# Performance work log

Hardware: AMD Instinct MI355X
Metric: run time of the kernel (lower is better)

Reference implementation:

```python
import jax, jax.numpy as jnp
import numpy as np

K = 4      # tagset_size - 2 (real emotion tags)
NT = 6     # tagset_size
START = 4
STOP = 5


def setup_inputs() -> dict:
    key = jax.random.key(0)
    ks = jax.random.split(key, 10)
    B, T = 2048, 2048
    feats = jax.random.normal(ks[0], (B, T, NT), dtype=jnp.float32)
    bias = jax.random.uniform(ks[1], (B, T), dtype=jnp.float32)        # bias_dict values in [0,1)
    tags = jax.random.randint(ks[2], (B, T), 0, K)                     # emotion labels only
    transitions = jax.random.normal(ks[3], (NT, NT), dtype=jnp.float32)
    transitions = transitions.at[START, :].set(-10000.0)
    transitions = transitions.at[:, STOP].set(-10000.0)
    w_shift_in = jax.random.normal(ks[4], (K,), dtype=jnp.float32)
    bias_no = jax.random.normal(ks[5], (1,), dtype=jnp.float32)
    bias_with = jax.random.normal(ks[6], (1,), dtype=jnp.float32)
    w_with_out = jax.random.normal(ks[7], (K,), dtype=jnp.float32)
    w_no_out = jax.random.normal(ks[8], (K,), dtype=jnp.float32)
    multiplier = jax.random.normal(ks[9], (K, K), dtype=jnp.float32)
    multiplier = multiplier.at[jnp.arange(K), jnp.arange(K)].set(-10000.0)
    return dict(feats=feats, bias=bias, tags=tags, transitions=transitions,
                w_shift_in=w_shift_in, bias_no=bias_no, bias_with=bias_with,
                w_with_out=w_with_out, w_no_out=w_no_out, multiplier=multiplier)


def reference(feats, bias, tags, transitions, w_shift_in, bias_no, bias_with,
              w_with_out, w_no_out, multiplier):
    """Batched neg_log_likelihood = forward_alg(feats) - score_sentence(feats, tags)."""
    B, T, _ = feats.shape
    # multiplier_softmax is over dim=0 (columns); diagonal overwritten with -1
    Mmod = jax.nn.softmax(multiplier, axis=0)
    Mmod = Mmod.at[jnp.arange(K), jnp.arange(K)].set(-1.0)

    # per-step transition gate, shape [B,T,K]; branch on bias > 0.5
    b = bias[..., None]
    gates = jnp.where(b > 0.5,
                      w_with_out * jnp.tanh(b * w_shift_in + bias_with),
                      w_no_out * jnp.tanh(b * w_shift_in + bias_no))

    # ---- forward algorithm (log-sum-exp DP over T, vectorized over B) ----
    init = jnp.full((B, NT), -10000.0, dtype=feats.dtype).at[:, START].set(0.0)
    feats_t = jnp.swapaxes(feats, 0, 1)   # [T,B,NT]
    gates_t = jnp.swapaxes(gates, 0, 1)   # [T,B,K]

    def step(alpha, x):
        f, g = x                                          # [B,NT], [B,K]
        blk = g[:, None, :] * Mmod[None, :, :]            # gate[prev] * Mmod[next,prev]
        Teff = transitions[None] + jnp.pad(blk, ((0, 0), (0, 2), (0, 2)))  # [B,NT,NT]
        alpha_new = f + jax.nn.logsumexp(alpha[:, None, :] + Teff, axis=2)
        return alpha_new, None

    alpha, _ = jax.lax.scan(step, init, (feats_t, gates_t))
    fwd_score = jax.nn.logsumexp(alpha + transitions[STOP][None, :], axis=1)  # [B]

    # ---- gold path score ----
    tags_ext = jnp.concatenate(
        [jnp.full((B, 1), START, dtype=tags.dtype), tags], axis=1)
    t0 = tags_ext[:, :-1]   # prev tag, [B,T]
    t1 = tags_ext[:, 1:]    # next tag, [B,T]
    base = transitions[t1, t0]
    Mext = jnp.pad(Mmod, ((0, 2), (0, 2)))
    gate_t0 = jnp.take_along_axis(gates, jnp.clip(t0, 0, K - 1)[..., None], axis=2)[..., 0]
    extra = jnp.where((t0 < K) & (t1 < K), gate_t0 * Mext[t1, t0], 0.0)
    emit = jnp.take_along_axis(feats, t1[..., None], axis=2)[..., 0]
    gold = jnp.sum(base + extra + emit, axis=1) + transitions[STOP, tags[:, -1]]

    return fwd_score - gold  # [B] per-dialog NLL
```

## Files before the change

### kernel.cpp

```cpp
#include <hip/hip_runtime.h>

#define BN 2048
#define TN 2048
#define BATCH 8
#define SLOT 24

__device__ __forceinline__ float ex2(float x){ return __builtin_amdgcn_exp2f(x); }
__device__ __forceinline__ float lg2(float x){ return __builtin_amdgcn_logf(x); }
__device__ __forceinline__ float rcpf(float x){ return __builtin_amdgcn_rcpf(x); }

constexpr float kLog2e = 1.4426950408889634f;
constexpr float kLn2   = 0.6931471805599453f;

__device__ __forceinline__ float fast_tanh(float x){
    float ax = fabsf(x);
    float e  = ex2(ax * (-2.0f * kLog2e));
    float t  = (1.0f - e) * rcpf(1.0f + e);
    return copysignf(t, x);
}

__device__ __forceinline__ float sel4(float v0, float v1, float v2, float v3, int idx){
    float r = (idx == 1) ? v1 : v0;
    r = (idx == 2) ? v2 : r;
    r = (idx == 3) ? v3 : r;
    return r;
}

template <int NCOL, bool CHUNK0, int TCH>
__device__ __forceinline__ void run_chunk(
    int b, int c,
    const float* __restrict__ feats, const float* __restrict__ bias,
    const int* __restrict__ tags,
    const float (&AL)[4][4], const float (&M)[4][4],
    const float (&wsv)[4], const float (&wwv)[4], const float (&wnv)[4],
    float bwc, float bnc, const float* sA, const float* sM,
    const float (&tc4)[4],
    float (&P)[4][NCOL], float (&lacc)[NCOL], float& gold, int& prev)
{
    const int t0c = c * TCH;
    #pragma unroll 1
    for (int bt = 0; bt < TCH / BATCH; ++bt) {
        const int t0 = t0c + bt * BATCH;
        float Fr[BATCH * 6];
        {
            const float4* fp4 = (const float4*)(feats + ((size_t)b * TN + t0) * 6);
            #pragma unroll
            for (int q = 0; q < BATCH * 6 / 4; ++q) {
                const float4 v = fp4[q];
                Fr[q*4+0] = v.x; Fr[q*4+1] = v.y; Fr[q*4+2] = v.z; Fr[q*4+3] = v.w;
            }
        }
        float Bv[BATCH];
        {
            const float4* bp4 = (const float4*)(bias + (size_t)b * TN + t0);
            #pragma unroll
            for (int q = 0; q < BATCH / 4; ++q) {
                const float4 v = bp4[q];
                Bv[q*4+0] = v.x; Bv[q*4+1] = v.y; Bv[q*4+2] = v.z; Bv[q*4+3] = v.w;
            }
        }
        int Tg[BATCH];
        {
            const int4* tp4 = (const int4*)(tags + (size_t)b * TN + t0);
            #pragma unroll
            for (int q = 0; q < BATCH / 4; ++q) {
                const int4 v = tp4[q];
                Tg[q*4+0] = v.x; Tg[q*4+1] = v.y; Tg[q*4+2] = v.z; Tg[q*4+3] = v.w;
            }
        }
        #pragma unroll
        for (int s = 0; s < BATCH; ++s) {
            const float fi0 = Fr[s*6+0], fi1 = Fr[s*6+1];
            const float fi2 = Fr[s*6+2], fi3 = Fr[s*6+3];
            if (CHUNK0 && bt == 0 && s == 0) {
                const float a0 = fi0 + tc4[0], a1 = fi1 + tc4[1];
                const float a2 = fi2 + tc4[2], a3 = fi3 + tc4[3];
                const float mx = fmaxf(fmaxf(a0, a1), fmaxf(a2, a3));
                P[0][0] = ex2((a0 - mx) * kLog2e);
                P[1][0] = ex2((a1 - mx) * kLog2e);
                P[2][0] = ex2((a2 - mx) * kLog2e);
                P[3][0] = ex2((a3 - mx) * kLog2e);
                lacc[0] = mx * kLog2e;
                const int tg0 = Tg[0];
                gold = sel4(tc4[0], tc4[1], tc4[2], tc4[3], tg0)
                     + sel4(fi0, fi1, fi2, fi3, tg0);
                prev = tg0;
                continue;
            }
            const float bv = Bv[s];
            const int tg = Tg[s];
            const bool hw = bv > 0.5f;
            const float bc = hw ? bwc : bnc;
            float g[4], gL[4];
            #pragma unroll
            for (int j = 0; j < 4; ++j) {
                float x = fmaf(bv, wsv[j], bc);
                g[j]  = (hw ? wwv[j] : wnv[j]) * fast_tanh(x);
                gL[j] = g[j] * kLog2e;
            }
            const float fiL[4] = { fi0 * kLog2e, fi1 * kLog2e,
                                   fi2 * kLog2e, fi3 * kLog2e };
            float nP[4][NCOL];
            #pragma unroll
            for (int i = 0; i < 4; ++i)
                #pragma unroll
                for (int j = 0; j < NCOL; ++j) nP[i][j] = 0.0f;
            #pragma unroll
            for (int k = 0; k < 4; ++k) {
                float Ek[4];
                #pragma unroll
                for (int i = 0; i < 4; ++i)
                    Ek[i] = ex2(fmaf(gL[k], M[i][k], fiL[i] + AL[i][k]));
                #pragma unroll
                for (int j = 0; j < NCOL; ++j) {
                    const float pk = P[k][j];
                    #pragma unroll
                    for (int i = 0; i < 4; ++i) nP[i][j] = fmaf(Ek[i], pk, nP[i][j]);
                }
            }
            #pragma unroll
            for (int i = 0; i < 4; ++i)
                #pragma unroll
                for (int j = 0; j < NCOL; ++j) P[i][j] = nP[i][j];

            const int idx = tg * 4 + prev;
            gold += sA[idx] + sel4(g[0], g[1], g[2], g[3], prev) * sM[idx]
                  + sel4(fi0, fi1, fi2, fi3, tg);
            prev = tg;

            if ((s & 3) == 3) {
                #pragma unroll
                for (int j = 0; j < NCOL; ++j) {
                    float m = fmaxf(fmaxf(P[0][j], P[1][j]), fmaxf(P[2][j], P[3][j]));
                    int ee = (int)((__float_as_uint(m) >> 23) & 255u) - 126;
                    float sc = __uint_as_float((unsigned)(127 - ee) << 23);
                    lacc[j] += (float)ee;
                    #pragma unroll
                    for (int i = 0; i < 4; ++i) P[i][j] *= sc;
                }
            }
        }
    }
}

template <int CCv>
__global__ void __launch_bounds__(256)
crf_phase1(const float* __restrict__ feats, const float* __restrict__ bias,
           const int* __restrict__ tags, const float* __restrict__ trans,
           const float* __restrict__ wsh, const float* __restrict__ bno,
           const float* __restrict__ bwi, const float* __restrict__ wwo,
           const float* __restrict__ wno, const float* __restrict__ mult,
           float* __restrict__ matAll)
{
    constexpr int TCHv = TN / CCv;
    constexpr int BPB  = 256 / CCv;
    const int b = blockIdx.x * BPB + (threadIdx.x / CCv);
    const int c = threadIdx.x % CCv;

    __shared__ float sA[16], sM[16];
    if (threadIdx.x < 16) {
        const int i = threadIdx.x >> 2, j = threadIdx.x & 3;
        sA[threadIdx.x] = trans[i * 6 + j];
        const float m0 = mult[j], m1 = mult[4 + j], m2 = mult[8 + j], m3 = mult[12 + j];
        const float mx = fmaxf(fmaxf(m0, m1), fmaxf(m2, m3));
        const float e0 = ex2((m0 - mx) * kLog2e), e1 = ex2((m1 - mx) * kLog2e);
        const float e2 = ex2((m2 - mx) * kLog2e), e3 = ex2((m3 - mx) * kLog2e);
        const float inv = rcpf(e0 + e1 + e2 + e3);
        const float ei = (i == 0) ? e0 : (i == 1) ? e1 : (i == 2) ? e2 : e3;
        sM[threadIdx.x] = (i == j) ? -1.0f : ei * inv;
    }
    __syncthreads();

    float AL[4][4], M[4][4];
    #pragma unroll
    for (int i = 0; i < 4; ++i)
        #pragma unroll
        for (int j = 0; j < 4; ++j) {
            AL[i][j] = trans[i * 6 + j] * kLog2e;
            M[i][j]  = sM[i * 4 + j];
        }
    float wsv[4], wwv[4], wnv[4];
    #pragma unroll
    for (int j = 0; j < 4; ++j) { wsv[j] = wsh[j]; wwv[j] = wwo[j]; wnv[j] = wno[j]; }
    const float bwc = bwi[0], bnc = bno[0];
    const float tc4[4] = { trans[4], trans[10], trans[16], trans[22] };

    float o[SLOT];
    float gold = 0.0f;
    int prev;
    if (c == 0) {
        float P[4][1], lacc[1];
        run_chunk<1, true, TCHv>(b, 0, feats, bias, tags, AL, M, wsv, wwv, wnv,
                                 bwc, bnc, sA, sM, tc4, P, lacc, gold, prev);
        #pragma unroll
        for (int i = 0; i < 4; ++i)
            #pragma unroll
            for (int j = 0; j < 4; ++j) o[i * 4 + j] = P[i][0];
        #pragma unroll
        for (int j = 0; j < 4; ++j) o[16 + j] = lacc[0];
    } else {
        float P[4][4], lacc[4] = {0.f, 0.f, 0.f, 0.f};
        #pragma unroll
        for (int i = 0; i < 4; ++i)
            #pragma unroll
            for (int j = 0; j < 4; ++j) P[i][j] = (i == j) ? 1.0f : 0.0f;
        prev = tags[(size_t)b * TN + c * TCHv - 1];
        run_chunk<4, false, TCHv>(b, c, feats, bias, tags, AL, M, wsv, wwv, wnv,
                                  bwc, bnc, sA, sM, tc4, P, lacc, gold, prev);
        #pragma unroll
        for (int i = 0; i < 4; ++i)
            #pragma unroll
            for (int j = 0; j < 4; ++j) o[i * 4 + j] = P[i][j];
        #pragma unroll
        for (int j = 0; j < 4; ++j) o[16 + j] = lacc[j];
    }
    o[20] = gold; o[21] = 0.f; o[22] = 0.f; o[23] = 0.f;
    float4* s4 = (float4*)(matAll + ((size_t)b * CCv + c) * SLOT);
    #pragma unroll
    for (int q = 0; q < SLOT / 4; ++q)
        s4[q] = make_float4(o[4*q], o[4*q+1], o[4*q+2], o[4*q+3]);
}

__device__ __forceinline__ void compose4(
    const float (&Ae)[4][4], const float (&sa)[4],
    const float (&Be)[4][4], const float (&sb)[4],
    float (&Ce)[4][4], float (&sc)[4])
{
    const float maxA = fmaxf(fmaxf(sa[0], sa[1]), fmaxf(sa[2], sa[3]));
    float Ap[4][4];
    #pragma unroll
    for (int k = 0; k < 4; ++k) {
        const float wk = ex2(sa[k] - maxA);
        #pragma unroll
        for (int i = 0; i < 4; ++i) Ap[i][k] = Ae[i][k] * wk;
    }
    #pragma unroll
    for (int j = 0; j < 4; ++j) {
        float c0 = 0.f, c1 = 0.f, c2 = 0.f, c3 = 0.f;
        #pragma unroll
        for (int k = 0; k < 4; ++k) {
            const float bk = Be[k][j];
            c0 = fmaf(Ap[0][k], bk, c0);
            c1 = fmaf(Ap[1][k], bk, c1);
            c2 = fmaf(Ap[2][k], bk, c2);
            c3 = fmaf(Ap[3][k], bk, c3);
        }
        const float m = fmaxf(fmaxf(c0, c1), fmaxf(c2, c3));
        const int ee = (int)((__float_as_uint(m) >> 23) & 255u) - 126;
        const float scf = __uint_as_float((unsigned)(127 - ee) << 23);
        Ce[0][j] = c0 * scf; Ce[1][j] = c1 * scf;
        Ce[2][j] = c2 * scf; Ce[3][j] = c3 * scf;
        sc[j] = sb[j] + maxA + (float)ee;
    }
}

template <int CCv>
__global__ void __launch_bounds__(256)
crf_phase2(const float* __restrict__ matAll, const float* __restrict__ trans,
           const int* __restrict__ tags, float* __restrict__ out)
{
    constexpr int CPL = CCv / 64;
    const int gtid = blockIdx.x * 256 + threadIdx.x;
    const int b = gtid >> 6;
    const int lane = threadIdx.x & 63;

    const float4* base = (const float4*)(matAll + ((size_t)b * CCv + lane * CPL) * SLOT);
    float Pe[4][4], so[4], gold;
    {
        float A[SLOT];
        #pragma unroll
        for (int q = 0; q < SLOT / 4; ++q) {
            const float4 v = base[q];
            A[4*q] = v.x; A[4*q+1] = v.y; A[4*q+2] = v.z; A[4*q+3] = v.w;
        }
        #pragma unroll
        for (int i = 0; i < 4; ++i)
            #pragma unroll
            for (int j = 0; j < 4; ++j) Pe[i][j] = A[i * 4 + j];
        #pragma unroll
        for (int j = 0; j < 4; ++j) so[j] = A[16 + j];
        gold = A[20];
    }
    #pragma unroll
    for (int p = 1; p < CPL; ++p) {
        float A[SLOT];
        #pragma unroll
        for (int q = 0; q < SLOT / 4; ++q) {
            const float4 v = base[p * (SLOT / 4) + q];
            A[4*q] = v.x; A[4*q+1] = v.y; A[4*q+2] = v.z; A[4*q+3] = v.w;
        }
        float Ae[4][4], sa[4];
        #pragma unroll
        for (int i = 0; i < 4; ++i)
            #pragma unroll
            for (int j = 0; j < 4; ++j) Ae[i][j] = A[i * 4 + j];
        #pragma unroll
        for (int j = 0; j < 4; ++j) sa[j] = A[16 + j];
        gold += A[20];
        float Ce[4][4], sc[4];
        compose4(Ae, sa, Pe, so, Ce, sc);
        #pragma unroll
        for (int i = 0; i < 4; ++i)
            #pragma unroll
            for (int j = 0; j < 4; ++j) Pe[i][j] = Ce[i][j];
        #pragma unroll
        for (int j = 0; j < 4; ++j) so[j] = sc[j];
    }

    #pragma unroll
    for (int d = 1; d < 64; d <<= 1) {
        float oP[4][4], os[4];
        #pragma unroll
        for (int i = 0; i < 4; ++i)
            #pragma unroll
            for (int j = 0; j < 4; ++j) oP[i][j] = __shfl_xor(Pe[i][j], d, 64);
        #pragma unroll
        for (int j = 0; j < 4; ++j) os[j] = __shfl_xor(so[j], d, 64);
        const bool hi = (lane & d) != 0;
        float Ae[4][4], Be[4][4], sa[4], sb[4];
        #pragma unroll
        for (int i = 0; i < 4; ++i)
            #pragma unroll
            for (int j = 0; j < 4; ++j) {
                Ae[i][j] = hi ? Pe[i][j] : oP[i][j];
                Be[i][j] = hi ? oP[i][j] : Pe[i][j];
            }
        #pragma unroll
        for (int j = 0; j < 4; ++j) {
            sa[j] = hi ? so[j] : os[j];
            sb[j] = hi ? os[j] : so[j];
        }
        float Ce[4][4], sc[4];
        compose4(Ae, sa, Be, sb, Ce, sc);
        #pragma unroll
        for (int i = 0; i < 4; ++i)
            #pragma unroll
            for (int j = 0; j < 4; ++j) Pe[i][j] = Ce[i][j];
        #pragma unroll
        for (int j = 0; j < 4; ++j) so[j] = sc[j];
    }

    #pragma unroll
    for (int d = 1; d < 64; d <<= 1) gold += __shfl_xor(gold, d, 64);

    if (lane == 0) {
        const float t50 = trans[30], t51 = trans[31], t52 = trans[32], t53 = trans[33];
        const float ssum = Pe[0][0] * ex2(t50 * kLog2e) + Pe[1][0] * ex2(t51 * kLog2e)
                         + Pe[2][0] * ex2(t52 * kLog2e) + Pe[3][0] * ex2(t53 * kLog2e);
        const float fwd = (so[0] + lg2(ssum)) * kLn2;
        const int lastT = tags[(size_t)b * TN + TN - 1];
        const float gfin = gold + sel4(t50, t51, t52, t53, lastT);
        out[b] = fwd - gfin;
    }
}

extern "C" void kernel_launch(void* const* d_in, const int* in_sizes, int n_in,
                              void* d_out, int out_size, void* d_ws, size_t ws_size,
                              hipStream_t stream)
{
    const float* feats = (const float*)d_in[0];
    const float* bias  = (const float*)d_in[1];
    const int*   tags  = (const int*)d_in[2];
    const float* trans = (const float*)d_in[3];
    const float* wsh   = (const float*)d_in[4];
    const float* bno   = (const float*)d_in[5];
    const float* bwi   = (const float*)d_in[6];
    const float* wwo   = (const float*)d_in[7];
    const float* wno   = (const float*)d_in[8];
    const float* mult  = (const float*)d_in[9];
    float* out = (float*)d_out;
    float* matAll = (float*)d_ws;

    const size_t need256 = (size_t)BN * 256 * SLOT * sizeof(float);
    const size_t need128 = (size_t)BN * 128 * SLOT * sizeof(float);
    if (ws_size >= need256) {
        crf_phase1<256><<<(256 * BN) / 256, 256, 0, stream>>>(
            feats, bias, tags, trans, wsh, bno, bwi, wwo, wno, mult, matAll);
        crf_phase2<256><<<(BN * 64) / 256, 256, 0, stream>>>(matAll, trans, tags, out);
    } else if (ws_size >= need128) {
        crf_phase1<128><<<(128 * BN) / 256, 256, 0, stream>>>(
            feats, bias, tags, trans, wsh, bno, bwi, wwo, wno, mult, matAll);
        crf_phase2<128><<<(BN * 64) / 256, 256, 0, stream>>>(matAll, trans, tags, out);
    } else {
        crf_phase1<64><<<(64 * BN) / 256, 256, 0, stream>>>(
            feats, bias, tags, trans, wsh, bno, bwi, wwo, wno, mult, matAll);
        crf_phase2<64><<<(BN * 64) / 256, 256, 0, stream>>>(matAll, trans, tags, out);
    }
}
```

Before: 219.3 us.

## Stage feats via global_load_lds, transpose matAll layout, single-block-per-batch phase 2

Phase 1 now stages each wave's contiguous feats window into LDS with direct global-to-LDS loads, so the global reads are coalesced. Each thread then reads its own 8-step slice from LDS instead of issuing strided per-thread float4 loads. The matAll intermediate is stored column-major per batch (slot-major, thread-minor) for coalesced writes and reads. Phase 2 uses one block per batch row with a wave-level shuffle scan plus a cross-wave LDS combine. It also sets launch bounds for 3 blocks per CU, adding LDS pressure and more complex indexing in exchange for better memory coalescing.

```diff
diff --git a/kernel.cpp b/kernel.cpp
--- a/kernel.cpp
+++ b/kernel.cpp
@@ -2,7 +2,6 @@
 
 #define BN 2048
 #define TN 2048
-#define BATCH 8
 #define SLOT 24
 
 __device__ __forceinline__ float ex2(float x){ return __builtin_amdgcn_exp2f(x); }
@@ -26,55 +25,91 @@
     return r;
 }
 
-template <int NCOL, bool CHUNK0, int TCH>
-__device__ __forceinline__ void run_chunk(
-    int b, int c,
-    const float* __restrict__ feats, const float* __restrict__ bias,
-    const int* __restrict__ tags,
-    const float (&AL)[4][4], const float (&M)[4][4],
-    const float (&wsv)[4], const float (&wwv)[4], const float (&wnv)[4],
-    float bwc, float bnc, const float* sA, const float* sM,
-    const float (&tc4)[4],
+__device__ __forceinline__ void gload_lds16(const void* g, void* l) {
+    __builtin_amdgcn_global_load_lds(
+        (const __attribute__((address_space(1))) void*)g,
+        (__attribute__((address_space(3))) void*)l, 16, 0, 0);
+}
+
+struct P1Params {
+    float AL[4][4], M[4][4];
+    float wsv[4], wwv[4], wnv[4];
+    float bwc, bnc;
+    const float* sA; const float* sM;
+    float tc4[4];
+};
+
+template <int NCOL>
+__device__ __forceinline__ void step_generic(
+    const P1Params& pp, float fi0, float fi1, float fi2, float fi3,
+    float bv, int tg, bool renorm,
     float (&P)[4][NCOL], float (&lacc)[NCOL], float& gold, int& prev)
 {
-    const int t0c = c * TCH;
-    #pragma unroll 1
-    for (int bt = 0; bt < TCH / BATCH; ++bt) {
-        const int t0 = t0c + bt * BATCH;
-        float Fr[BATCH * 6];
+    const bool hw = bv > 0.5f;
+    const float bc = hw ? pp.bwc : pp.bnc;
+    float g[4], gL[4];
+    #pragma unroll
+    for (int j = 0; j < 4; ++j) {
+        float x = fmaf(bv, pp.wsv[j], bc);
+        g[j]  = (hw ? pp.wwv[j] : pp.wnv[j]) * fast_tanh(x);
+        gL[j] = g[j] * kLog2e;
+    }
+    const float fiL[4] = { fi0 * kLog2e, fi1 * kLog2e, fi2 * kLog2e, fi3 * kLog2e };
+    float nP[4][NCOL];
+    #pragma unroll
+    for (int i = 0; i < 4; ++i)
+        #pragma unroll
+        for (int j = 0; j < NCOL; ++j) nP[i][j] = 0.0f;
+    #pragma unroll
+    for (int k = 0; k < 4; ++k) {
+        float Ek[4];
+        #pragma unroll
+        for (int i = 0; i < 4; ++i)
+            Ek[i] = ex2(fmaf(gL[k], pp.M[i][k], fiL[i] + pp.AL[i][k]));
+        #pragma unroll
+        for (int j = 0; j < NCOL; ++j) {
+            const float pk = P[k][j];
+            #pragma unroll
+            for (int i = 0; i < 4; ++i) nP[i][j] = fmaf(Ek[i], pk, nP[i][j]);
+        }
+    }
+    #pragma unroll
+    for (int i = 0; i < 4; ++i)
+        #pragma unroll
+        for (int j = 0; j < NCOL; ++j) P[i][j] = nP[i][j];
+
+    const int idx = tg * 4 + prev;
+    gold += pp.sA[idx] + sel4(g[0], g[1], g[2], g[3], prev) * pp.sM[idx]
+          + sel4(fi0, fi1, fi2, fi3, tg);
+    prev = tg;
+
+    if (renorm) {
+        #pragma unroll
+        for (int j = 0; j < NCOL; ++j) {
+            float m = fmaxf(fmaxf(P[0][j], P[1][j]), fmaxf(P[2][j], P[3][j]));
+            int ee = (int)((__float_as_uint(m) >> 23) & 255u) - 126;
+            float sc = __uint_as_float((unsigned)(127 - ee) << 23);
+            lacc[j] += (float)ee;
+            #pragma unroll
+            for (int i = 0; i < 4; ++i) P[i][j] *= sc;
+        }
+    }
+}
+
+template <int NCOL, bool C0>
+__device__ __forceinline__ void trip8(
+    const float4* myF, const float (&Bv)[8], const int (&Tg)[8],
+    const P1Params& pp,
+    float (&P)[4][NCOL], float (&lacc)[NCOL], float& gold, int& prev)
+{
+    #pragma unroll
+    for (int p = 0; p < 4; ++p) {
+        const float4 fA = myF[3*p], fB = myF[3*p+1], fC = myF[3*p+2];
         {
-            const float4* fp4 = (const float4*)(feats + ((size_t)b * TN + t0) * 6);
-            #pragma unroll
-            for (int q = 0; q < BATCH * 6 / 4; ++q) {
-                const float4 v = fp4[q];
-                Fr[q*4+0] = v.x; Fr[q*4+1] = v.y; Fr[q*4+2] = v.z; Fr[q*4+3] = v.w;
-            }
-        }
-        float Bv[BATCH];
-        {
-            const float4* bp4 = (const float4*)(bias + (size_t)b * TN + t0);
-            #pragma unroll
-            for (int q = 0; q < BATCH / 4; ++q) {
-                const float4 v = bp4[q];
-                Bv[q*4+0] = v.x; Bv[q*4+1] = v.y; Bv[q*4+2] = v.z; Bv[q*4+3] = v.w;
-            }
-        }
-        int Tg[BATCH];
-        {
-            const int4* tp4 = (const int4*)(tags + (size_t)b * TN + t0);
-            #pragma unroll
-            for (int q = 0; q < BATCH / 4; ++q) {
-                const int4 v = tp4[q];
-                Tg[q*4+0] = v.x; Tg[q*4+1] = v.y; Tg[q*4+2] = v.z; Tg[q*4+3] = v.w;
-            }
-        }
-        #pragma unroll
-        for (int s = 0; s < BATCH; ++s) {
-            const float fi0 = Fr[s*6+0], fi1 = Fr[s*6+1];
-            const float fi2 = Fr[s*6+2], fi3 = Fr[s*6+3];
-            if (CHUNK0 && bt == 0 && s == 0) {
-                const float a0 = fi0 + tc4[0], a1 = fi1 + tc4[1];
-                const float a2 = fi2 + tc4[2], a3 = fi3 + tc4[3];
+            const float fi0 = fA.x, fi1 = fA.y, fi2 = fA.z, fi3 = fA.w;
+            if (C0 && p == 0) {
+                const float a0 = fi0 + pp.tc4[0], a1 = fi1 + pp.tc4[1];
+                const float a2 = fi2 + pp.tc4[2], a3 = fi3 + pp.tc4[3];
                 const float mx = fmaxf(fmaxf(a0, a1), fmaxf(a2, a3));
                 P[0][0] = ex2((a0 - mx) * kLog2e);
                 P[1][0] = ex2((a1 - mx) * kLog2e);
@@ -82,75 +117,332 @@
                 P[3][0] = ex2((a3 - mx) * kLog2e);
                 lacc[0] = mx * kLog2e;
                 const int tg0 = Tg[0];
-                gold = sel4(tc4[0], tc4[1], tc4[2], tc4[3], tg0)
+                gold = sel4(pp.tc4[0], pp.tc4[1], pp.tc4[2], pp.tc4[3], tg0)
+                     + sel4(fi0, fi1, fi2, fi3, tg0);
+                prev = tg0;
+            } else {
+                step_generic<NCOL>(pp, fi0, fi1, fi2, fi3, Bv[2*p], Tg[2*p],
+                                   ((2*p) & 3) == 3, P, lacc, gold, prev);
+            }
+        }
+        {
+            const float fi0 = fB.z, fi1 = fB.w, fi2 = fC.x, fi3 = fC.y;
+            step_generic<NCOL>(pp, fi0, fi1, fi2, fi3, Bv[2*p+1], Tg[2*p+1],
+                               ((2*p+1) & 3) == 3, P, lacc, gold, prev);
+        }
+    }
+}
+
+__global__ void __launch_bounds__(256, 3)
+crf_phase1_t(const float* __restrict__ feats, const float* __restrict__ bias,
+             const int* __restrict__ tags, const float* __restrict__ trans,
+             const float* __restrict__ wsh, const float* __restrict__ bno,
+             const float* __restrict__ bwi, const float* __restrict__ wwo,
+             const float* __restrict__ wno, const float* __restrict__ mult,
+             float* __restrict__ matAll)
+{
+    constexpr int CC = 256, TCH = 8;
+    const int w = threadIdx.x >> 6;
+    const int L = threadIdx.x & 63;
+    const int b = blockIdx.x;
+    const int c = threadIdx.x;
+
+    __shared__ float4 ldsA[4][13 * 64];
+    __shared__ float sA[16], sM[16];
+    float4* ldsW = ldsA[w];
+
+    {
+        const float4* gwin4 = (const float4*)(feats + ((size_t)b * TN + (size_t)w * 64 * TCH) * 6);
+        #pragma unroll
+        for (int q = 0; q < 13; ++q) {
+            const int S  = q * 64 + L;
+            const int cS = (S * 2521) >> 15;
+            int j = S - cS * 13;
+            j = (j > 11) ? 11 : j;
+            gload_lds16(gwin4 + cS * 12 + j, &ldsW[q * 64]);
+        }
+    }
+
+    float Bv[8]; int Tg[8];
+    {
+        const int tbase = c * TCH;
+        const float4* bp = (const float4*)(bias + (size_t)b * TN + tbase);
+        const float4 b0 = bp[0], b1 = bp[1];
+        Bv[0]=b0.x; Bv[1]=b0.y; Bv[2]=b0.z; Bv[3]=b0.w;
+        Bv[4]=b1.x; Bv[5]=b1.y; Bv[6]=b1.z; Bv[7]=b1.w;
+        const int4* tp = (const int4*)(tags + (size_t)b * TN + tbase);
+        const int4 t0 = tp[0], t1 = tp[1];
+        Tg[0]=t0.x; Tg[1]=t0.y; Tg[2]=t0.z; Tg[3]=t0.w;
+        Tg[4]=t1.x; Tg[5]=t1.y; Tg[6]=t1.z; Tg[7]=t1.w;
+    }
+    int prev = 0;
+    if (c != 0) prev = tags[(size_t)b * TN + c * TCH - 1];
+
+    if (threadIdx.x < 16) {
+        const int i = threadIdx.x >> 2, j = threadIdx.x & 3;
+        sA[threadIdx.x] = trans[i * 6 + j];
+        const float m0 = mult[j], m1 = mult[4 + j], m2 = mult[8 + j], m3 = mult[12 + j];
+        const float mx = fmaxf(fmaxf(m0, m1), fmaxf(m2, m3));
+        const float e0 = ex2((m0 - mx) * kLog2e), e1 = ex2((m1 - mx) * kLog2e);
+        const float e2 = ex2((m2 - mx) * kLog2e), e3 = ex2((m3 - mx) * kLog2e);
+        const float inv = rcpf(e0 + e1 + e2 + e3);
+        const float ei = (i == 0) ? e0 : (i == 1) ? e1 : (i == 2) ? e2 : e3;
+        sM[threadIdx.x] = (i == j) ? -1.0f : ei * inv;
+    }
+    __syncthreads();
+    asm volatile("s_waitcnt vmcnt(0)" ::: "memory");
+
+    P1Params pp;
+    #pragma unroll
+    for (int i = 0; i < 4; ++i)
+        #pragma unroll
+        for (int j = 0; j < 4; ++j) {
+            pp.AL[i][j] = trans[i * 6 + j] * kLog2e;
+            pp.M[i][j]  = sM[i * 4 + j];
+        }
+    #pragma unroll
+    for (int j = 0; j < 4; ++j) { pp.wsv[j] = wsh[j]; pp.wwv[j] = wwo[j]; pp.wnv[j] = wno[j]; }
+    pp.bwc = bwi[0]; pp.bnc = bno[0];
+    pp.sA = sA; pp.sM = sM;
+    pp.tc4[0] = trans[4]; pp.tc4[1] = trans[10]; pp.tc4[2] = trans[16]; pp.tc4[3] = trans[22];
+
+    const float4* myF = &ldsW[L * 13];
+
+    float o[SLOT];
+    float gold = 0.0f;
+    if (c == 0) {
+        float P[4][1], lacc[1];
+        trip8<1, true>(myF, Bv, Tg, pp, P, lacc, gold, prev);
+        #pragma unroll
+        for (int i = 0; i < 4; ++i)
+            #pragma unroll
+            for (int j = 0; j < 4; ++j) o[i * 4 + j] = P[i][0];
+        #pragma unroll
+        for (int j = 0; j < 4; ++j) o[16 + j] = lacc[0];
+    } else {
+        float P[4][4], lacc[4] = {0.f, 0.f, 0.f, 0.f};
+        #pragma unroll
+        for (int i = 0; i < 4; ++i)
+            #pragma unroll
+            for (int j = 0; j < 4; ++j) P[i][j] = (i == j) ? 1.0f : 0.0f;
+        trip8<4, false>(myF, Bv, Tg, pp, P, lacc, gold, prev);
+        #pragma unroll
+        for (int i = 0; i < 4; ++i)
+            #pragma unroll
+            for (int j = 0; j < 4; ++j) o[i * 4 + j] = P[i][j];
+        #pragma unroll
+        for (int j = 0; j < 4; ++j) o[16 + j] = lacc[j];
+    }
+    o[20] = gold; o[21] = 0.f; o[22] = 0.f; o[23] = 0.f;
+
+    float4* mp = (float4*)matAll + (size_t)b * 6 * CC;
+    #pragma unroll
+    for (int q = 0; q < 6; ++q)
+        mp[q * CC + c] = make_float4(o[4*q], o[4*q+1], o[4*q+2], o[4*q+3]);
+}
+
+__device__ __forceinline__ void compose4(
+    const float (&Ae)[4][4], const float (&sa)[4],
+    const float (&Be)[4][4], const float (&sb)[4],
+    float (&Ce)[4][4], float (&sc)[4])
+{
+    const float maxA = fmaxf(fmaxf(sa[0], sa[1]), fmaxf(sa[2], sa[3]));
+    float Ap[4][4];
+    #pragma unroll
+    for (int k = 0; k < 4; ++k) {
+        const float wk = ex2(sa[k] - maxA);
+        #pragma unroll
+        for (int i = 0; i < 4; ++i) Ap[i][k] = Ae[i][k] * wk;
+    }
+    #pragma unroll
+    for (int j = 0; j < 4; ++j) {
+        float c0 = 0.f, c1 = 0.f, c2 = 0.f, c3 = 0.f;
+        #pragma unroll
+        for (int k = 0; k < 4; ++k) {
+            const float bk = Be[k][j];
+            c0 = fmaf(Ap[0][k], bk, c0);
+            c1 = fmaf(Ap[1][k], bk, c1);
+            c2 = fmaf(Ap[2][k], bk, c2);
+            c3 = fmaf(Ap[3][k], bk, c3);
+        }
+        const float m = fmaxf(fmaxf(c0, c1), fmaxf(c2, c3));
+        const int ee = (int)((__float_as_uint(m) >> 23) & 255u) - 126;
+        const float scf = __uint_as_float((unsigned)(127 - ee) << 23);
+        Ce[0][j] = c0 * scf; Ce[1][j] = c1 * scf;
+        Ce[2][j] = c2 * scf; Ce[3][j] = c3 * scf;
+        sc[j] = sb[j] + maxA + (float)ee;
+    }
+}
+
+__global__ void __launch_bounds__(256)
+crf_phase2_t(const float* __restrict__ matAll, const float* __restrict__ trans,
+             const int* __restrict__ tags, float* __restrict__ out)
+{
+    constexpr int CC = 256;
+    const int b = blockIdx.x;
+    const int c = threadIdx.x;
+    const int L = c & 63, w = c >> 6;
+
+    const float4* mp = (const float4*)matAll + (size_t)b * 6 * CC;
+    float4 v[6];
+    #pragma unroll
+    for (int q = 0; q < 6; ++q) v[q] = mp[q * CC + c];
+
+    float Pe[4][4], so[4], gold;
+    #pragma unroll
+    for (int i = 0; i < 4; ++i) {
+        Pe[i][0] = (&v[i].x)[0]; Pe[i][1] = (&v[i].x)[1];
+        Pe[i][2] = (&v[i].x)[2]; Pe[i][3] = (&v[i].x)[3];
+    }
+    so[0] = v[4].x; so[1] = v[4].y; so[2] = v[4].z; so[3] = v[4].w;
+    gold = v[5].x;
+
+    #pragma unroll
+    for (int d = 1; d < 64; d <<= 1) {
+        float oP[4][4], os[4];
+        #pragma unroll
+        for (int i = 0; i < 4; ++i)
+            #pragma unroll
+            for (int j = 0; j < 4; ++j) oP[i][j] = __shfl_xor(Pe[i][j], d, 64);
+        #pragma unroll
+        for (int j = 0; j < 4; ++j) os[j] = __shfl_xor(so[j], d, 64);
+        const bool hi = (L & d) != 0;
+        float Ae[4][4], Be[4][4], sa[4], sb[4];
+        #pragma unroll
+        for (int i = 0; i < 4; ++i)
+            #pragma unroll
+            for (int j = 0; j < 4; ++j) {
+                Ae[i][j] = hi ? Pe[i][j] : oP[i][j];
+                Be[i][j] = hi ? oP[i][j] : Pe[i][j];
+            }
+        #pragma unroll
+        for (int j = 0; j < 4; ++j) {
+            sa[j] = hi ? so[j] : os[j];
+            sb[j] = hi ? os[j] : so[j];
+        }
+        float Ce[4][4], sc[4];
+        compose4(Ae, sa, Be, sb, Ce, sc);
+        #pragma unroll
+        for (int i = 0; i < 4; ++i)
+            #pragma unroll
+            for (int j = 0; j < 4; ++j) Pe[i][j] = Ce[i][j];
+        #pragma unroll
+        for (int j = 0; j < 4; ++j) so[j] = sc[j];
+    }
+    #pragma unroll
+    for (int d = 1; d < 64; d <<= 1) gold += __shfl_xor(gold, d, 64);
+
+    __shared__ float red[4][24];
+    if (L == 0) {
+        #pragma unroll
+        for (int i = 0; i < 4; ++i)
+            #pragma unroll
+            for (int j = 0; j < 4; ++j) red[w][i * 4 + j] = Pe[i][j];
+        #pragma unroll
+        for (int j = 0; j < 4; ++j) red[w][16 + j] = so[j];
+        red[w][20] = gold;
+    }
+    __syncthreads();
+    if (threadIdx.x == 0) {
+        float Pt[4][4], st[4];
+        #pragma unroll
+        for (int i = 0; i < 4; ++i)
+            #pragma unroll
+            for (int j = 0; j < 4; ++j) Pt[i][j] = red[0][i * 4 + j];
+        #pragma unroll
+        for (int j = 0; j < 4; ++j) st[j] = red[0][16 + j];
+        float gsum = red[0][20] + red[1][20] + red[2][20] + red[3][20];
+        #pragma unroll
+        for (int ww = 1; ww < 4; ++ww) {
+            float Ae[4][4], sa[4], Ce[4][4], scv[4];
+            #pragma unroll
+            for (int i = 0; i < 4; ++i)
+                #pragma unroll
+                for (int j = 0; j < 4; ++j) Ae[i][j] = red[ww][i * 4 + j];
+            #pragma unroll
+            for (int j = 0; j < 4; ++j) sa[j] = red[ww][16 + j];
+            compose4(Ae, sa, Pt, st, Ce, scv);
+            #pragma unroll
+            for (int i = 0; i < 4; ++i)
+                #pragma unroll
+                for (int j = 0; j < 4; ++j) Pt[i][j] = Ce[i][j];
+            #pragma unroll
+            for (int j = 0; j < 4; ++j) st[j] = scv[j];
+        }
+        const float t50 = trans[30], t51 = trans[31], t52 = trans[32], t53 = trans[33];
+        const float ssum = Pt[0][0] * ex2(t50 * kLog2e) + Pt[1][0] * ex2(t51 * kLog2e)
+                         + Pt[2][0] * ex2(t52 * kLog2e) + Pt[3][0] * ex2(t53 * kLog2e);
+        const float fwd = (st[0] + lg2(ssum)) * kLn2;
+        const int lastT = tags[(size_t)b * TN + TN - 1];
+        const float gfin = gsum + sel4(t50, t51, t52, t53, lastT);
+        out[b] = fwd - gfin;
+    }
+}
+
+template <int NCOL, bool CHUNK0, int TCH>
+__device__ __forceinline__ void run_chunk_fb(
+    int b, int c,
+    const float* __restrict__ feats, const float* __restrict__ bias,
+    const int* __restrict__ tags, const P1Params& pp,
+    float (&P)[4][NCOL], float (&lacc)[NCOL], float& gold, int& prev)
+{
+    const int t0c = c * TCH;
+    #pragma unroll 1
+    for (int bt = 0; bt < TCH / 8; ++bt) {
+        const int t0 = t0c + bt * 8;
+        float Fr[48];
+        {
+            const float4* fp4 = (const float4*)(feats + ((size_t)b * TN + t0) * 6);
+            #pragma unroll
+            for (int q = 0; q < 12; ++q) {
+                const float4 vv = fp4[q];
+                Fr[q*4+0] = vv.x; Fr[q*4+1] = vv.y; Fr[q*4+2] = vv.z; Fr[q*4+3] = vv.w;
+            }
+        }
+        float Bv[8]; int Tg[8];
+        {
+            const float4* bp4 = (const float4*)(bias + (size_t)b * TN + t0);
+            const float4 v0 = bp4[0], v1 = bp4[1];
+            Bv[0]=v0.x; Bv[1]=v0.y; Bv[2]=v0.z; Bv[3]=v0.w;
+            Bv[4]=v1.x; Bv[5]=v1.y; Bv[6]=v1.z; Bv[7]=v1.w;
+            const int4* tp4 = (const int4*)(tags + (size_t)b * TN + t0);
+            const int4 u0 = tp4[0], u1 = tp4[1];
+            Tg[0]=u0.x; Tg[1]=u0.y; Tg[2]=u0.z; Tg[3]=u0.w;
+            Tg[4]=u1.x; Tg[5]=u1.y; Tg[6]=u1.z; Tg[7]=u1.w;
+        }
+        #pragma unroll
+        for (int s = 0; s < 8; ++s) {
+            const float fi0 = Fr[s*6+0], fi1 = Fr[s*6+1];
+            const float fi2 = Fr[s*6+2], fi3 = Fr[s*6+3];
+            if (CHUNK0 && bt == 0 && s == 0) {
+                const float a0 = fi0 + pp.tc4[0], a1 = fi1 + pp.tc4[1];
+                const float a2 = fi2 + pp.tc4[2], a3 = fi3 + pp.tc4[3];
+                const float mx = fmaxf(fmaxf(a0, a1), fmaxf(a2, a3));
+                P[0][0] = ex2((a0 - mx) * kLog2e);
+                P[1][0] = ex2((a1 - mx) * kLog2e);
+                P[2][0] = ex2((a2 - mx) * kLog2e);
+                P[3][0] = ex2((a3 - mx) * kLog2e);
+                lacc[0] = mx * kLog2e;
+                const int tg0 = Tg[0];
+                gold = sel4(pp.tc4[0], pp.tc4[1], pp.tc4[2], pp.tc4[3], tg0)
                      + sel4(fi0, fi1, fi2, fi3, tg0);
                 prev = tg0;
                 continue;
             }
-            const float bv = Bv[s];
-            const int tg = Tg[s];
-            const bool hw = bv > 0.5f;
-            const float bc = hw ? bwc : bnc;
-            float g[4], gL[4];
-            #pragma unroll
-            for (int j = 0; j < 4; ++j) {
-                float x = fmaf(bv, wsv[j], bc);
-                g[j]  = (hw ? wwv[j] : wnv[j]) * fast_tanh(x);
-                gL[j] = g[j] * kLog2e;
-            }
-            const float fiL[4] = { fi0 * kLog2e, fi1 * kLog2e,
-                                   fi2 * kLog2e, fi3 * kLog2e };
-            float nP[4][NCOL];
-            #pragma unroll
-            for (int i = 0; i < 4; ++i)
-                #pragma unroll
-                for (int j = 0; j < NCOL; ++j) nP[i][j] = 0.0f;
-            #pragma unroll
-            for (int k = 0; k < 4; ++k) {
-                float Ek[4];
-                #pragma unroll
-                for (int i = 0; i < 4; ++i)
-                    Ek[i] = ex2(fmaf(gL[k], M[i][k], fiL[i] + AL[i][k]));
-                #pragma unroll
-                for (int j = 0; j < NCOL; ++j) {
-                    const float pk = P[k][j];
-                    #pragma unroll
-                    for (int i = 0; i < 4; ++i) nP[i][j] = fmaf(Ek[i], pk, nP[i][j]);
-                }
-            }
-            #pragma unroll
-            for (int i = 0; i < 4; ++i)
-                #pragma unroll
-                for (int j = 0; j < NCOL; ++j) P[i][j] = nP[i][j];
-
-            const int idx = tg * 4 + prev;
-            gold += sA[idx] + sel4(g[0], g[1], g[2], g[3], prev) * sM[idx]
-                  + sel4(fi0, fi1, fi2, fi3, tg);
-            prev = tg;
-
-            if ((s & 3) == 3) {
-                #pragma unroll
-                for (int j = 0; j < NCOL; ++j) {
-                    float m = fmaxf(fmaxf(P[0][j], P[1][j]), fmaxf(P[2][j], P[3][j]));
-                    int ee = (int)((__float_as_uint(m) >> 23) & 255u) - 126;
-                    float sc = __uint_as_float((unsigned)(127 - ee) << 23);
-                    lacc[j] += (float)ee;
-                    #pragma unroll
-                    for (int i = 0; i < 4; ++i) P[i][j] *= sc;
-                }
-            }
+            step_generic<NCOL>(pp, fi0, fi1, fi2, fi3, Bv[s], Tg[s],
+                               (s & 3) == 3, P, lacc, gold, prev);
         }
     }
 }
 
 template <int CCv>
 __global__ void __launch_bounds__(256)
-crf_phase1(const float* __restrict__ feats, const float* __restrict__ bias,
-           const int* __restrict__ tags, const float* __restrict__ trans,
-           const float* __restrict__ wsh, const float* __restrict__ bno,
-           const float* __restrict__ bwi, const float* __restrict__ wwo,
-           const float* __restrict__ wno, const float* __restrict__ mult,
-           float* __restrict__ matAll)
+crf_phase1_fb(const float* __restrict__ feats, const float* __restrict__ bias,
+              const int* __restrict__ tags, const float* __restrict__ trans,
+              const float* __restrict__ wsh, const float* __restrict__ bno,
+              const float* __restrict__ bwi, const float* __restrict__ wwo,
+              const float* __restrict__ wno, const float* __restrict__ mult,
+              float* __restrict__ matAll)
 {
     constexpr int TCHv = TN / CCv;
     constexpr int BPB  = 256 / CCv;
@@ -171,27 +463,26 @@
     }
     __syncthreads();
 
-    float AL[4][4], M[4][4];
+    P1Params pp;
     #pragma unroll
     for (int i = 0; i < 4; ++i)
         #pragma unroll
         for (int j = 0; j < 4; ++j) {
-            AL[i][j] = trans[i * 6 + j] * kLog2e;
-            M[i][j]  = sM[i * 4 + j];
-        }
-    float wsv[4], wwv[4], wnv[4];
-    #pragma unroll
-    for (int j = 0; j < 4; ++j) { wsv[j] = wsh[j]; wwv[j] = wwo[j]; wnv[j] = wno[j]; }
-    const float bwc = bwi[0], bnc = bno[0];
-    const float tc4[4] = { trans[4], trans[10], trans[16], trans[22] };
+            pp.AL[i][j] = trans[i * 6 + j] * kLog2e;
+            pp.M[i][j]  = sM[i * 4 + j];
+        }
+    #pragma unroll
+    for (int j = 0; j < 4; ++j) { pp.wsv[j] = wsh[j]; pp.wwv[j] = wwo[j]; pp.wnv[j] = wno[j]; }
+    pp.bwc = bwi[0]; pp.bnc = bno[0];
+    pp.sA = sA; pp.sM = sM;
+    pp.tc4[0] = trans[4]; pp.tc4[1] = trans[10]; pp.tc4[2] = trans[16]; pp.tc4[3] = trans[22];
 
     float o[SLOT];
     float gold = 0.0f;
     int prev;
     if (c == 0) {
         float P[4][1], lacc[1];
-        run_chunk<1, true, TCHv>(b, 0, feats, bias, tags, AL, M, wsv, wwv, wnv,
-                                 bwc, bnc, sA, sM, tc4, P, lacc, gold, prev);
+        run_chunk_fb<1, true, TCHv>(b, 0, feats, bias, tags, pp, P, lacc, gold, prev);
         #pragma unroll
         for (int i = 0; i < 4; ++i)
             #pragma unroll
@@ -205,8 +496,7 @@
             #pragma unroll
             for (int j = 0; j < 4; ++j) P[i][j] = (i == j) ? 1.0f : 0.0f;
         prev = tags[(size_t)b * TN + c * TCHv - 1];
-        run_chunk<4, false, TCHv>(b, c, feats, bias, tags, AL, M, wsv, wwv, wnv,
-                                  bwc, bnc, sA, sM, tc4, P, lacc, gold, prev);
+        run_chunk_fb<4, false, TCHv>(b, c, feats, bias, tags, pp, P, lacc, gold, prev);
         #pragma unroll
         for (int i = 0; i < 4; ++i)
             #pragma unroll
@@ -221,43 +511,10 @@
         s4[q] = make_float4(o[4*q], o[4*q+1], o[4*q+2], o[4*q+3]);
 }
 
-__device__ __forceinline__ void compose4(
-    const float (&Ae)[4][4], const float (&sa)[4],
-    const float (&Be)[4][4], const float (&sb)[4],
-    float (&Ce)[4][4], float (&sc)[4])
-{
-    const float maxA = fmaxf(fmaxf(sa[0], sa[1]), fmaxf(sa[2], sa[3]));
-    float Ap[4][4];
-    #pragma unroll
-    for (int k = 0; k < 4; ++k) {
-        const float wk = ex2(sa[k] - maxA);
-        #pragma unroll
-        for (int i = 0; i < 4; ++i) Ap[i][k] = Ae[i][k] * wk;
-    }
-    #pragma unroll
-    for (int j = 0; j < 4; ++j) {
-        float c0 = 0.f, c1 = 0.f, c2 = 0.f, c3 = 0.f;
-        #pragma unroll
-        for (int k = 0; k < 4; ++k) {
-            const float bk = Be[k][j];
-            c0 = fmaf(Ap[0][k], bk, c0);
-            c1 = fmaf(Ap[1][k], bk, c1);
-            c2 = fmaf(Ap[2][k], bk, c2);
-            c3 = fmaf(Ap[3][k], bk, c3);
-        }
-        const float m = fmaxf(fmaxf(c0, c1), fmaxf(c2, c3));
-        const int ee = (int)((__float_as_uint(m) >> 23) & 255u) - 126;
-        const float scf = __uint_as_float((unsigned)(127 - ee) << 23);
-        Ce[0][j] = c0 * scf; Ce[1][j] = c1 * scf;
-        Ce[2][j] = c2 * scf; Ce[3][j] = c3 * scf;
-        sc[j] = sb[j] + maxA + (float)ee;
-    }
-}
-
 template <int CCv>
 __global__ void __launch_bounds__(256)
-crf_phase2(const float* __restrict__ matAll, const float* __restrict__ trans,
-           const int* __restrict__ tags, float* __restrict__ out)
+crf_phase2_fb(const float* __restrict__ matAll, const float* __restrict__ trans,
+              const int* __restrict__ tags, float* __restrict__ out)
 {
     constexpr int CPL = CCv / 64;
     const int gtid = blockIdx.x * 256 + threadIdx.x;
@@ -374,16 +631,16 @@
     const size_t need256 = (size_t)BN * 256 * SLOT * sizeof(float);
     const size_t need128 = (size_t)BN * 128 * SLOT * sizeof(float);
     if (ws_size >= need256) {
-        crf_phase1<256><<<(256 * BN) / 256, 256, 0, stream>>>(
+        crf_phase1_t<<<BN, 256, 0, stream>>>(
             feats, bias, tags, trans, wsh, bno, bwi, wwo, wno, mult, matAll);
-        crf_phase2<256><<<(BN * 64) / 256, 256, 0, stream>>>(matAll, trans, tags, out);
+        crf_phase2_t<<<BN, 256, 0, stream>>>(matAll, trans, tags, out);
     } else if (ws_size >= need128) {
-        crf_phase1<128><<<(128 * BN) / 256, 256, 0, stream>>>(
+        crf_phase1_fb<128><<<(128 * BN) / 256, 256, 0, stream>>>(
             feats, bias, tags, trans, wsh, bno, bwi, wwo, wno, mult, matAll);
-        crf_phase2<128><<<(BN * 64) / 256, 256, 0, stream>>>(matAll, trans, tags, out);
+        crf_phase2_fb<128><<<(BN * 64) / 256, 256, 0, stream>>>(matAll, trans, tags, out);
     } else {
-        crf_phase1<64><<<(64 * BN) / 256, 256, 0, stream>>>(
+        crf_phase1_fb<64><<<(64 * BN) / 256, 256, 0, stream>>>(
             feats, bias, tags, trans, wsh, bno, bwi, wwo, wno, mult, matAll);
-        crf_phase2<64><<<(BN * 64) / 256, 256, 0, stream>>>(matAll, trans, tags, out);
-    }
-}
+        crf_phase2_fb<64><<<(BN * 64) / 256, 256, 0, stream>>>(matAll, trans, tags, out);
+    }
+}
```

Measured after the change: 354.4 us. +61.6%, slower.
